# Kernel tuning notes

Hardware: AMD Instinct MI355X
Metric: run time of the kernel (lower is better)

## Reference

```python
import jax, jax.numpy as jnp
import numpy as np

NUM_USERS = 100000
NUM_ITEMS = 50000
N_NODES = NUM_USERS + NUM_ITEMS
EMB = 64          # emb_dim == layers[0]
NNZ = 2_400_000   # ~16 avg degree normalized-Laplacian nonzeros
BATCH = 16384


def spmm(rows, cols, vals, x, n):
    # sparse (COO) Laplacian @ dense features: out[r] += v * x[c]
    return jax.ops.segment_sum(vals[:, None] * x[cols], rows, num_segments=n)


def setup_inputs() -> dict:
    key = jax.random.key(0)
    ks = jax.random.split(key, 20)
    userIdx = jax.random.randint(ks[0], (BATCH,), 0, NUM_USERS)
    itemIdx = jax.random.randint(ks[1], (BATCH,), 0, NUM_ITEMS)
    lap_rows = jax.random.randint(ks[2], (NNZ,), 0, N_NODES, dtype=jnp.int32)
    lap_cols = jax.random.randint(ks[3], (NNZ,), 0, N_NODES, dtype=jnp.int32)
    # normalized Laplacian values ~ 1/sqrt(deg_i*deg_j), small positive
    lap_vals = jax.random.uniform(ks[4], (NNZ,), dtype=jnp.float32) * 0.05
    uEmb = jax.random.normal(ks[5], (NUM_USERS, EMB), dtype=jnp.float32) * 0.1
    iEmb = jax.random.normal(ks[6], (NUM_ITEMS, EMB), dtype=jnp.float32) * 0.1
    s = 1.0 / np.sqrt(EMB)
    gW0 = jax.random.normal(ks[7], (EMB, EMB), dtype=jnp.float32) * s
    gb0 = jnp.zeros((EMB,), jnp.float32)
    gW1 = jax.random.normal(ks[8], (EMB, EMB), dtype=jnp.float32) * s
    gb1 = jnp.zeros((EMB,), jnp.float32)
    D_CAT = EMB * 3 * 2  # 384
    W1 = jax.random.normal(ks[9], (D_CAT, 64), dtype=jnp.float32) / np.sqrt(D_CAT)
    b1 = jnp.zeros((64,), jnp.float32)
    W2 = jax.random.normal(ks[10], (64, 32), dtype=jnp.float32) / 8.0
    b2 = jnp.zeros((32,), jnp.float32)
    W3 = jax.random.normal(ks[11], (32, 1), dtype=jnp.float32) / np.sqrt(32.0)
    b3 = jnp.zeros((1,), jnp.float32)
    return {"userIdx": userIdx, "itemIdx": itemIdx,
            "lap_rows": lap_rows, "lap_cols": lap_cols, "lap_vals": lap_vals,
            "uEmb": uEmb, "iEmb": iEmb,
            "gW0": gW0, "gb0": gb0, "gW1": gW1, "gb1": gb1,
            "W1": W1, "b1": b1, "W2": W2, "b2": b2, "W3": W3, "b3": b3}


def reference(userIdx, itemIdx, lap_rows, lap_cols, lap_vals,
              uEmb, iEmb, gW0, gb0, gW1, gb1, W1, b1, W2, b2, W3, b3):
    features = jnp.concatenate([uEmb, iEmb], axis=0)  # [N, EMB]
    final = features
    for W, b in ((gW0, gb0), (gW1, gb1)):
        # (Laplacian + selfLoop I) @ features, then linear + ReLU
        h = spmm(lap_rows, lap_cols, lap_vals, features, N_NODES) + features
        features = jax.nn.relu(h @ W + b)
        final = jnp.concatenate([final, features], axis=1)
    u = final[userIdx]                     # [B, 192]
    it = final[itemIdx + NUM_USERS]        # [B, 192]
    e = jnp.concatenate([u, it], axis=1)   # [B, 384]
    e = jax.nn.relu(e @ W1 + b1)
    e = e @ W2 + b2
    e = e @ W3 + b3
    return e.ravel()
```

## Files before the change

### kernel.cpp

```cpp
#include <hip/hip_runtime.h>
#include <hip/hip_bf16.h>

#define NUM_USERS 100000
#define NUM_ITEMS 50000
#define N_NODES   150000
#define EMB       64
#define NNZ       2400000
#define BATCH     16384
#define D_CAT     384
#define BSHIFT    8
#define NBUCK     ((N_NODES + 255) >> 8)
#define EPB       9375

__device__ __forceinline__ unsigned short f2bf(float f) {
    unsigned u = __float_as_uint(f);
    unsigned r = u + 0x7fffu + ((u >> 16) & 1u);
    return (unsigned short)(r >> 16);
}
__device__ __forceinline__ float bflo(unsigned u) { return __uint_as_float(u << 16); }
__device__ __forceinline__ float bfhi(unsigned u) { return __uint_as_float(u & 0xffff0000u); }

__global__ __launch_bounds__(1024) void bucket_hist(const int* __restrict__ rows,
                                                    int* __restrict__ bcnt, int nnz) {
    __shared__ int h[NBUCK];
    int tid = threadIdx.x;
    for (int i = tid; i < NBUCK; i += 1024) h[i] = 0;
    __syncthreads();
    for (int i = blockIdx.x * 1024 + tid; i < nnz; i += gridDim.x * 1024)
        atomicAdd(&h[rows[i] >> BSHIFT], 1);
    __syncthreads();
    for (int i = tid; i < NBUCK; i += 1024) {
        int c = h[i];
        if (c) atomicAdd(&bcnt[i], c);
    }
}

__global__ __launch_bounds__(1024) void bucket_scan(const int* __restrict__ bcnt,
                                                    int* __restrict__ boffs,
                                                    int* __restrict__ gtails, int nnz) {
    __shared__ int s[1024];
    int t = threadIdx.x;
    int x = (t < NBUCK) ? bcnt[t] : 0;
    s[t] = x;
    __syncthreads();
#pragma unroll
    for (int off = 1; off < 1024; off <<= 1) {
        int v = (t >= off) ? s[t - off] : 0;
        __syncthreads();
        s[t] += v;
        __syncthreads();
    }
    if (t < NBUCK) {
        int e = s[t] - x;
        boffs[t] = e;
        gtails[t] = e;
    }
    if (t == 0) boffs[NBUCK] = nnz;
}

__global__ __launch_bounds__(1024) void coarse_multisplit(const int* __restrict__ rows,
                                                          const int* __restrict__ cols,
                                                          const float* __restrict__ vals,
                                                          int* __restrict__ gtails,
                                                          int2* __restrict__ pv, int nnz) {
    extern __shared__ int dyn[];
    int2* stage = (int2*)dyn;
    int*  smap  = dyn + 2 * EPB;
    __shared__ int hcnt[NBUCK];
    __shared__ int lstart[NBUCK];
    __shared__ int shiftv[NBUCK];

    int tid = threadIdx.x;
    int e0 = blockIdx.x * EPB;
    int e1 = e0 + EPB < nnz ? e0 + EPB : nnz;
    int nE = e1 - e0;

    for (int i = tid; i < NBUCK; i += 1024) hcnt[i] = 0;
    __syncthreads();
    for (int i = e0 + tid; i < e1; i += 1024)
        atomicAdd(&hcnt[rows[i] >> BSHIFT], 1);
    __syncthreads();

    int cnt = (tid < NBUCK) ? hcnt[tid] : 0;
    smap[tid] = cnt;
    __syncthreads();
#pragma unroll
    for (int off = 1; off < 1024; off <<= 1) {
        int v = (tid >= off) ? smap[tid - off] : 0;
        __syncthreads();
        smap[tid] += v;
        __syncthreads();
    }
    if (tid < NBUCK) {
        int ls = smap[tid] - cnt;
        lstart[tid] = ls;
        hcnt[tid] = ls;
        int gb = cnt ? atomicAdd(&gtails[tid], cnt) : 0;
        shiftv[tid] = gb - ls;
    }
    __syncthreads();

    for (int b = tid; b < NBUCK; b += 1024) {
        int beg = lstart[b];
        int end_ = (b == NBUCK - 1) ? nE : lstart[b + 1];
        int sh = shiftv[b];
        for (int k = beg; k < end_; ++k) smap[k] = sh;
    }
    __syncthreads();

    for (int i = e0 + tid; i < e1; i += 1024) {
        int r = rows[i];
        int p = atomicAdd(&hcnt[r >> BSHIFT], 1);
        stage[p] = make_int2(((r & 255) << 18) | cols[i], __float_as_int(vals[i]));
    }
    __syncthreads();

    for (int j = tid; j < nE; j += 1024)
        pv[smap[j] + j] = stage[j];
}

__global__ __launch_bounds__(1024) void fine_scatter(const int* __restrict__ boffs,
                                                     const int2* __restrict__ pv,
                                                     int2* __restrict__ packed,
                                                     int* __restrict__ row_ptr, int nnz) {
    __shared__ int rcnt[256];
    __shared__ int loff[256];
    int b = blockIdx.x;
    int tid = threadIdx.x;
    int lo = boffs[b], hi = boffs[b + 1];
    int r0 = b << BSHIFT;
    int nr = N_NODES - r0; if (nr > 256) nr = 256;

    if (tid < 256) rcnt[tid] = 0;
    __syncthreads();
    for (int i = lo + tid; i < hi; i += 1024)
        atomicAdd(&rcnt[pv[i].x >> 18], 1);
    __syncthreads();
    if (tid < 256) loff[tid] = rcnt[tid];
    __syncthreads();
#pragma unroll
    for (int off = 1; off < 256; off <<= 1) {
        int v = (tid < 256 && tid >= off) ? loff[tid - off] : 0;
        __syncthreads();
        if (tid < 256) loff[tid] += v;
        __syncthreads();
    }
    if (tid < 256) {
        int e = lo + loff[tid] - rcnt[tid];
        loff[tid] = e;
        if (tid < nr) row_ptr[r0 + tid] = e;
    }
    if (b == 0 && tid == 0) row_ptr[N_NODES] = nnz;
    __syncthreads();
    for (int i = lo + tid; i < hi; i += 1024) {
        int2 e = pv[i];
        int rl = e.x >> 18;
        int pos = atomicAdd(&loff[rl], 1);
        packed[pos] = make_int2(e.x & 0x3FFFF, e.y);
    }
}

__global__ __launch_bounds__(256) void gemm_table_f32(const float* __restrict__ uE,
                                                      const float* __restrict__ iE,
                                                      const float* __restrict__ W,
                                                      unsigned short* __restrict__ Zh,
                                                      int n_rows) {
    __shared__ float Wl[64 * 64];
    __shared__ float Xf[64 * 64];
    int tid = threadIdx.x;
    int lane = tid & 63;
    int wave = tid >> 6;
    int r0 = blockIdx.x * 64;
    int last = n_rows - 1;

    for (int i = tid; i < 64 * 64; i += 256) Wl[i] = W[i];
    for (int i = tid; i < 64 * 16; i += 256) {
        int row = i >> 4, q = i & 15;
        int r = r0 + row; r = r > last ? last : r;
        const float4* src = (r < NUM_USERS)
            ? (const float4*)(uE + (size_t)r * 64)
            : (const float4*)(iE + (size_t)(r - NUM_USERS) * 64);
        ((float4*)Xf)[i] = src[q];
    }
    __syncthreads();

    int rbase = wave * 16;
    float acc[16];
#pragma unroll
    for (int i = 0; i < 16; ++i) acc[i] = 0.f;

#pragma unroll 1
    for (int kc = 0; kc < 16; ++kc) {
        float w0 = Wl[(kc * 4 + 0) * 64 + lane];
        float w1 = Wl[(kc * 4 + 1) * 64 + lane];
        float w2 = Wl[(kc * 4 + 2) * 64 + lane];
        float w3 = Wl[(kc * 4 + 3) * 64 + lane];
#pragma unroll
        for (int i = 0; i < 16; ++i) {
            float4 q = ((const float4*)Xf)[(rbase + i) * 16 + kc];
            acc[i] = fmaf(q.x, w0, acc[i]);
            acc[i] = fmaf(q.y, w1, acc[i]);
            acc[i] = fmaf(q.z, w2, acc[i]);
            acc[i] = fmaf(q.w, w3, acc[i]);
        }
    }
#pragma unroll
    for (int i = 0; i < 16; ++i) {
        int r = r0 + rbase + i;
        if (r < n_rows) Zh[(size_t)r * 64 + lane] = f2bf(acc[i]);
    }
}

__global__ __launch_bounds__(256) void gemm_table_bf16(const unsigned* __restrict__ Xh,
                                                       const float* __restrict__ W,
                                                       unsigned short* __restrict__ Zh,
                                                       int n_rows) {
    __shared__ float Wl[64 * 64];
    __shared__ uint4 Xl4[64 * 8];
    int tid = threadIdx.x;
    int lane = tid & 63;
    int wave = tid >> 6;
    int r0 = blockIdx.x * 64;
    int nr = n_rows - r0; if (nr > 64) nr = 64;

    for (int i = tid; i < 64 * 64; i += 256) Wl[i] = W[i];
    const uint4* Xg4 = (const uint4*)(Xh + (size_t)r0 * 32);
    for (int i = tid; i < nr * 8; i += 256) Xl4[i] = Xg4[i];
    __syncthreads();

    const unsigned* Xl = (const unsigned*)Xl4;
    int rbase = wave * 16;
    float acc[16];
#pragma unroll
    for (int i = 0; i < 16; ++i) acc[i] = 0.f;

#pragma unroll 1
    for (int kc = 0; kc < 8; ++kc) {
        float w0 = Wl[(kc * 8 + 0) * 64 + lane];
        float w1 = Wl[(kc * 8 + 1) * 64 + lane];
        float w2 = Wl[(kc * 8 + 2) * 64 + lane];
        float w3 = Wl[(kc * 8 + 3) * 64 + lane];
        float w4 = Wl[(kc * 8 + 4) * 64 + lane];
        float w5 = Wl[(kc * 8 + 5) * 64 + lane];
        float w6 = Wl[(kc * 8 + 6) * 64 + lane];
        float w7 = Wl[(kc * 8 + 7) * 64 + lane];
#pragma unroll
        for (int i = 0; i < 16; ++i) {
            uint4 q = *(const uint4*)&Xl[(rbase + i) * 32 + kc * 4];
            acc[i] = fmaf(bflo(q.x), w0, acc[i]);
            acc[i] = fmaf(bfhi(q.x), w1, acc[i]);
            acc[i] = fmaf(bflo(q.y), w2, acc[i]);
            acc[i] = fmaf(bfhi(q.y), w3, acc[i]);
            acc[i] = fmaf(bflo(q.z), w4, acc[i]);
            acc[i] = fmaf(bfhi(q.z), w5, acc[i]);
            acc[i] = fmaf(bflo(q.w), w6, acc[i]);
            acc[i] = fmaf(bfhi(q.w), w7, acc[i]);
        }
    }
#pragma unroll
    for (int i = 0; i < 16; ++i) {
        int r = r0 + rbase + i;
        if (r < n_rows) Zh[(size_t)r * 64 + lane] = f2bf(acc[i]);
    }
}

__global__ __launch_bounds__(256) void spmm_bias_relu(const int* __restrict__ row_ptr,
                                                      const int2* __restrict__ packed,
                                                      const uint2* __restrict__ zh2,
                                                      const float* __restrict__ bias,
                                                      uint2* __restrict__ outh2,
                                                      int n_rows) {
    int tid = threadIdx.x;
    int lane = tid & 63;
    int wave = tid >> 6;
    int q = lane >> 4;
    int k = lane & 15;
    int r = blockIdx.x * 4 + wave;
    if (r >= n_rows) return;

    uint2 su = zh2[(size_t)r * 16 + k];
    float4 acc;
    acc.x = q ? 0.f : bflo(su.x);
    acc.y = q ? 0.f : bfhi(su.x);
    acc.z = q ? 0.f : bflo(su.y);
    acc.w = q ? 0.f : bfhi(su.y);

    int e = row_ptr[r] + q;
    int end = row_ptr[r + 1];
    for (; e + 13 < end; e += 16) {
        int2 p0 = packed[e + 0];
        int2 p1 = packed[e + 4];
        int2 p2 = packed[e + 8];
        int2 p3 = packed[e + 12];
        uint2 z0 = zh2[(size_t)p0.x * 16 + k];
        uint2 z1 = zh2[(size_t)p1.x * 16 + k];
        uint2 z2 = zh2[(size_t)p2.x * 16 + k];
        uint2 z3 = zh2[(size_t)p3.x * 16 + k];
        float v0 = __int_as_float(p0.y), v1 = __int_as_float(p1.y);
        float v2 = __int_as_float(p2.y), v3 = __int_as_float(p3.y);
        acc.x = fmaf(v0, bflo(z0.x), acc.x); acc.y = fmaf(v0, bfhi(z0.x), acc.y);
        acc.z = fmaf(v0, bflo(z0.y), acc.z); acc.w = fmaf(v0, bfhi(z0.y), acc.w);
        acc.x = fmaf(v1, bflo(z1.x), acc.x); acc.y = fmaf(v1, bfhi(z1.x), acc.y);
        acc.z = fmaf(v1, bflo(z1.y), acc.z); acc.w = fmaf(v1, bfhi(z1.y), acc.w);
        acc.x = fmaf(v2, bflo(z2.x), acc.x); acc.y = fmaf(v2, bfhi(z2.x), acc.y);
        acc.z = fmaf(v2, bflo(z2.y), acc.z); acc.w = fmaf(v2, bfhi(z2.y), acc.w);
        acc.x = fmaf(v3, bflo(z3.x), acc.x); acc.y = fmaf(v3, bfhi(z3.x), acc.y);
        acc.z = fmaf(v3, bflo(z3.y), acc.z); acc.w = fmaf(v3, bfhi(z3.y), acc.w);
    }
    for (; e < end; e += 4) {
        int2 p = packed[e];
        uint2 z = zh2[(size_t)p.x * 16 + k];
        float v = __int_as_float(p.y);
        acc.x = fmaf(v, bflo(z.x), acc.x); acc.y = fmaf(v, bfhi(z.x), acc.y);
        acc.z = fmaf(v, bflo(z.y), acc.z); acc.w = fmaf(v, bfhi(z.y), acc.w);
    }

    acc.x += __shfl_xor(acc.x, 16, 64);
    acc.y += __shfl_xor(acc.y, 16, 64);
    acc.z += __shfl_xor(acc.z, 16, 64);
    acc.w += __shfl_xor(acc.w, 16, 64);
    acc.x += __shfl_xor(acc.x, 32, 64);
    acc.y += __shfl_xor(acc.y, 32, 64);
    acc.z += __shfl_xor(acc.z, 32, 64);
    acc.w += __shfl_xor(acc.w, 32, 64);
    if (q == 0) {
        float4 bv = ((const float4*)bias)[k];
        float a = fmaxf(acc.x + bv.x, 0.f);
        float b = fmaxf(acc.y + bv.y, 0.f);
        float c = fmaxf(acc.z + bv.z, 0.f);
        float d = fmaxf(acc.w + bv.w, 0.f);
        outh2[(size_t)r * 16 + k] = make_uint2(
            ((unsigned)f2bf(b) << 16) | (unsigned)f2bf(a),
            ((unsigned)f2bf(d) << 16) | (unsigned)f2bf(c));
    }
}

__global__ __launch_bounds__(1024) void fused_mlp(
        const int* __restrict__ userIdx, const int* __restrict__ itemIdx,
        const float* __restrict__ uEmb, const float* __restrict__ iEmb,
        const unsigned short* __restrict__ feat1h,
        const unsigned short* __restrict__ feat2h,
        const float* __restrict__ W1, const float* __restrict__ b1,
        const float* __restrict__ W2, const float* __restrict__ b2,
        const float* __restrict__ W3, const float* __restrict__ b3,
        float* __restrict__ out) {
    __shared__ float    Wl[128 * 64];
    __shared__ unsigned El[64 * 64];
    __shared__ float    Ht[64 * 64];
    __shared__ float    W2l[64 * 32];
    __shared__ float    w3l[32];
    __shared__ float    b2l[32];
    __shared__ int      uidx[64], iidx[64];
    int tid = threadIdx.x;
    int lane = tid & 63;
    int wave = tid >> 6;
    int r0 = blockIdx.x * 64;
    int rbase = wave * 4;

    if (tid < 64) uidx[tid] = userIdx[r0 + tid];
    else if (tid < 128) iidx[tid - 64] = itemIdx[r0 + tid - 64];
    if (tid < 32) { w3l[tid] = W3[tid]; b2l[tid] = b2[tid]; }
    for (int i = tid; i < 64 * 32; i += 1024) W2l[i] = W2[i];

    float acc[4];
    float bv = b1[lane];
#pragma unroll
    for (int i = 0; i < 4; ++i) acc[i] = bv;

#pragma unroll 1
    for (int c = 0; c < 3; ++c) {
        __syncthreads();
        for (int i = tid; i < 128 * 64; i += 1024) Wl[i] = W1[c * 128 * 64 + i];
        {
            int t = tid;
            int row = t >> 4;
            int seg = (t >> 3) & 1;
            int q   = t & 7;
            int gseg = c * 2 + seg;
            uint4 val;
            if (gseg == 0 || gseg == 3) {
                const float* p = (gseg == 0)
                    ? uEmb + (size_t)uidx[row] * 64 + q * 8
                    : iEmb + (size_t)iidx[row] * 64 + q * 8;
                float4 a = *(const float4*)p;
                float4 b = *(const float4*)(p + 4);
                val.x = ((unsigned)f2bf(a.y) << 16) | f2bf(a.x);
                val.y = ((unsigned)f2bf(a.w) << 16) | f2bf(a.z);
                val.z = ((unsigned)f2bf(b.y) << 16) | f2bf(b.x);
                val.w = ((unsigned)f2bf(b.w) << 16) | f2bf(b.z);
            } else {
                const unsigned short* src;
                if (gseg == 1)      src = feat1h + (size_t)uidx[row] * 64;
                else if (gseg == 2) src = feat2h + (size_t)uidx[row] * 64;
                else if (gseg == 4) src = feat1h + (size_t)(iidx[row] + NUM_USERS) * 64;
                else                src = feat2h + (size_t)(iidx[row] + NUM_USERS) * 64;
                val = *(const uint4*)(src + q * 8);
            }
            *(uint4*)&El[row * 64 + seg * 32 + q * 4] = val;
        }
        __syncthreads();
        const uint4* El4 = (const uint4*)El;
#pragma unroll 1
        for (int k = 0; k < 128; k += 8) {
            float w0 = Wl[(k + 0) * 64 + lane];
            float w1 = Wl[(k + 1) * 64 + lane];
            float w2 = Wl[(k + 2) * 64 + lane];
            float w3 = Wl[(k + 3) * 64 + lane];
            float w4 = Wl[(k + 4) * 64 + lane];
            float w5 = Wl[(k + 5) * 64 + lane];
            float w6 = Wl[(k + 6) * 64 + lane];
            float w7 = Wl[(k + 7) * 64 + lane];
#pragma unroll
            for (int i = 0; i < 4; ++i) {
                uint4 q = El4[(rbase + i) * 16 + (k >> 3)];
                acc[i] = fmaf(bflo(q.x), w0, acc[i]);
                acc[i] = fmaf(bfhi(q.x), w1, acc[i]);
                acc[i] = fmaf(bflo(q.y), w2, acc[i]);
                acc[i] = fmaf(bfhi(q.y), w3, acc[i]);
                acc[i] = fmaf(bflo(q.z), w4, acc[i]);
                acc[i] = fmaf(bfhi(q.z), w5, acc[i]);
                acc[i] = fmaf(bflo(q.w), w6, acc[i]);
                acc[i] = fmaf(bfhi(q.w), w7, acc[i]);
            }
        }
    }

#pragma unroll
    for (int i = 0; i < 4; ++i) Ht[(rbase + i) * 64 + lane] = fmaxf(acc[i], 0.f);
    __syncthreads();

    int half = lane >> 5;
    int k = lane & 31;
    float b3v = b3[0];
#pragma unroll 1
    for (int p = 0; p < 2; ++p) {
        int row = rbase + p * 2 + half;
        float z = b2l[k];
#pragma unroll
        for (int j = 0; j < 64; ++j)
            z = fmaf(Ht[row * 64 + j], W2l[j * 32 + k], z);
        z *= w3l[k];
#pragma unroll
        for (int off = 16; off; off >>= 1)
            z += __shfl_xor(z, off, 64);
        if (k == 0) out[r0 + row] = z + b3v;
    }
}

extern "C" void kernel_launch(void* const* d_in, const int* in_sizes, int n_in,
                              void* d_out, int out_size, void* d_ws, size_t ws_size,
                              hipStream_t stream) {
    const int*   userIdx = (const int*)  d_in[0];
    const int*   itemIdx = (const int*)  d_in[1];
    const int*   lap_rows= (const int*)  d_in[2];
    const int*   lap_cols= (const int*)  d_in[3];
    const float* lap_vals= (const float*)d_in[4];
    const float* uEmb    = (const float*)d_in[5];
    const float* iEmb    = (const float*)d_in[6];
    const float* gW0     = (const float*)d_in[7];
    const float* gb0     = (const float*)d_in[8];
    const float* gW1     = (const float*)d_in[9];
    const float* gb1     = (const float*)d_in[10];
    const float* W1      = (const float*)d_in[11];
    const float* b1      = (const float*)d_in[12];
    const float* W2      = (const float*)d_in[13];
    const float* b2      = (const float*)d_in[14];
    const float* W3      = (const float*)d_in[15];
    const float* b3      = (const float*)d_in[16];
    float* out = (float*)d_out;

    const size_t NF = (size_t)N_NODES * EMB;
    char* w = (char*)d_ws;
    unsigned short* bufA = (unsigned short*)w;
    unsigned short* bufB = bufA + NF;
    char*  region3 = (char*)(bufB + NF);
    int2*  pv      = (int2*)region3;
    unsigned short* Zh = (unsigned short*)region3;
    int2*  packed  = (int2*)(region3 + NF * sizeof(float));
    int*   row_ptr = (int*)(packed + NNZ);
    int*   boffs   = row_ptr + (N_NODES + 1);
    int*   gtails  = boffs + (NBUCK + 1);
    int*   bcnt    = gtails + NBUCK;

    const int ms_grid   = (NNZ + EPB - 1) / EPB;
    const int ms_lds    = EPB * 12;
    const int spmm_grid = (N_NODES + 3) / 4;
    const int gemm_grid = (N_NODES + 63) / 64;

    hipMemsetAsync(bcnt, 0, NBUCK * sizeof(int), stream);
    bucket_hist<<<256, 1024, 0, stream>>>(lap_rows, bcnt, NNZ);
    bucket_scan<<<1, 1024, 0, stream>>>(bcnt, boffs, gtails, NNZ);
    coarse_multisplit<<<ms_grid, 1024, ms_lds, stream>>>(lap_rows, lap_cols, lap_vals,
                                                         gtails, pv, NNZ);
    fine_scatter<<<NBUCK, 1024, 0, stream>>>(boffs, pv, packed, row_ptr, NNZ);

    gemm_table_f32<<<gemm_grid, 256, 0, stream>>>(uEmb, iEmb, gW0, Zh, N_NODES);
    spmm_bias_relu<<<spmm_grid, 256, 0, stream>>>(row_ptr, packed, (const uint2*)Zh,
                                                  gb0, (uint2*)bufA, N_NODES);

    gemm_table_bf16<<<gemm_grid, 256, 0, stream>>>((const unsigned*)bufA, gW1, Zh, N_NODES);
    spmm_bias_relu<<<spmm_grid, 256, 0, stream>>>(row_ptr, packed, (const uint2*)Zh,
                                                  gb1, (uint2*)bufB, N_NODES);

    fused_mlp<<<BATCH / 64, 1024, 0, stream>>>(userIdx, itemIdx, uEmb, iEmb,
                                               bufA, bufB, W1, b1, W2, b2, W3, b3, out);
}
```

Before: 456.7 us.

## Fuse layer-1 SpMM epilogue with layer-2 dense transform into one kernel

Adds a kernel that runs the first SpMM with bias and ReLU, then immediately multiplies each output row by gW1 using register-held weights and readlane broadcasts, writing the next layer's Z table to a separate tail buffer. This removes the separate gemm_table_bf16 launch and its re-read of bufA. Each wave now processes 16 rows sequentially with 64 weight registers per thread, which lowers the number of waves in flight for the latency-bound gather. The fused path is used only when the workspace has room for the extra buffer.

Result: slower. 502.8 us (+10.1%).

```diff
diff --git a/kernel.cpp b/kernel.cpp
--- a/kernel.cpp
+++ b/kernel.cpp
@@ -332,6 +332,101 @@
         outh2[(size_t)r * 16 + k] = make_uint2(
             ((unsigned)f2bf(b) << 16) | (unsigned)f2bf(a),
             ((unsigned)f2bf(d) << 16) | (unsigned)f2bf(c));
+    }
+}
+
+__global__ __launch_bounds__(256) void spmm_bias_relu_z(const int* __restrict__ row_ptr,
+                                                        const int2* __restrict__ packed,
+                                                        const uint2* __restrict__ zh2,
+                                                        const float* __restrict__ bias,
+                                                        uint2* __restrict__ outh2,
+                                                        const float* __restrict__ Wz,
+                                                        unsigned short* __restrict__ Zh_out,
+                                                        int n_rows) {
+    int tid = threadIdx.x;
+    int lane = tid & 63;
+    int wave = tid >> 6;
+    int q = lane >> 4;
+    int k = lane & 15;
+
+    float wreg[64];
+#pragma unroll
+    for (int j = 0; j < 64; ++j) wreg[j] = Wz[j * 64 + lane];
+
+    float4 bv = ((const float4*)bias)[k];
+    int rbase = (blockIdx.x * 4 + wave) * 16;
+
+#pragma unroll 1
+    for (int ii = 0; ii < 16; ++ii) {
+        int r = rbase + ii;
+        if (r >= n_rows) break;
+
+        uint2 su = zh2[(size_t)r * 16 + k];
+        float4 acc;
+        acc.x = q ? 0.f : bflo(su.x);
+        acc.y = q ? 0.f : bfhi(su.x);
+        acc.z = q ? 0.f : bflo(su.y);
+        acc.w = q ? 0.f : bfhi(su.y);
+
+        int e = row_ptr[r] + q;
+        int end = row_ptr[r + 1];
+        for (; e + 13 < end; e += 16) {
+            int2 p0 = packed[e + 0];
+            int2 p1 = packed[e + 4];
+            int2 p2 = packed[e + 8];
+            int2 p3 = packed[e + 12];
+            uint2 z0 = zh2[(size_t)p0.x * 16 + k];
+            uint2 z1 = zh2[(size_t)p1.x * 16 + k];
+            uint2 z2 = zh2[(size_t)p2.x * 16 + k];
+            uint2 z3 = zh2[(size_t)p3.x * 16 + k];
+            float v0 = __int_as_float(p0.y), v1 = __int_as_float(p1.y);
+            float v2 = __int_as_float(p2.y), v3 = __int_as_float(p3.y);
+            acc.x = fmaf(v0, bflo(z0.x), acc.x); acc.y = fmaf(v0, bfhi(z0.x), acc.y);
+            acc.z = fmaf(v0, bflo(z0.y), acc.z); acc.w = fmaf(v0, bfhi(z0.y), acc.w);
+            acc.x = fmaf(v1, bflo(z1.x), acc.x); acc.y = fmaf(v1, bfhi(z1.x), acc.y);
+            acc.z = fmaf(v1, bflo(z1.y), acc.z); acc.w = fmaf(v1, bfhi(z1.y), acc.w);
+            acc.x = fmaf(v2, bflo(z2.x), acc.x); acc.y = fmaf(v2, bfhi(z2.x), acc.y);
+            acc.z = fmaf(v2, bflo(z2.y), acc.z); acc.w = fmaf(v2, bfhi(z2.y), acc.w);
+            acc.x = fmaf(v3, bflo(z3.x), acc.x); acc.y = fmaf(v3, bfhi(z3.x), acc.y);
+            acc.z = fmaf(v3, bflo(z3.y), acc.z); acc.w = fmaf(v3, bfhi(z3.y), acc.w);
+        }
+        for (; e < end; e += 4) {
+            int2 p = packed[e];
+            uint2 z = zh2[(size_t)p.x * 16 + k];
+            float v = __int_as_float(p.y);
+            acc.x = fmaf(v, bflo(z.x), acc.x); acc.y = fmaf(v, bfhi(z.x), acc.y);
+            acc.z = fmaf(v, bflo(z.y), acc.z); acc.w = fmaf(v, bfhi(z.y), acc.w);
+        }
+
+        acc.x += __shfl_xor(acc.x, 16, 64);
+        acc.y += __shfl_xor(acc.y, 16, 64);
+        acc.z += __shfl_xor(acc.z, 16, 64);
+        acc.w += __shfl_xor(acc.w, 16, 64);
+        acc.x += __shfl_xor(acc.x, 32, 64);
+        acc.y += __shfl_xor(acc.y, 32, 64);
+        acc.z += __shfl_xor(acc.z, 32, 64);
+        acc.w += __shfl_xor(acc.w, 32, 64);
+
+        float a = fmaxf(acc.x + bv.x, 0.f);
+        float b = fmaxf(acc.y + bv.y, 0.f);
+        float c = fmaxf(acc.z + bv.z, 0.f);
+        float d = fmaxf(acc.w + bv.w, 0.f);
+        int pa = (int)(((unsigned)f2bf(b) << 16) | (unsigned)f2bf(a));
+        int pb = (int)(((unsigned)f2bf(d) << 16) | (unsigned)f2bf(c));
+        if (q == 0)
+            outh2[(size_t)r * 16 + k] = make_uint2((unsigned)pa, (unsigned)pb);
+
+        float z = 0.f;
+#pragma unroll
+        for (int jj = 0; jj < 16; ++jj) {
+            unsigned ua = (unsigned)__builtin_amdgcn_readlane(pa, jj);
+            unsigned ub = (unsigned)__builtin_amdgcn_readlane(pb, jj);
+            z = fmaf(bflo(ua), wreg[4 * jj + 0], z);
+            z = fmaf(bfhi(ua), wreg[4 * jj + 1], z);
+            z = fmaf(bflo(ub), wreg[4 * jj + 2], z);
+            z = fmaf(bfhi(ub), wreg[4 * jj + 3], z);
+        }
+        Zh_out[(size_t)r * 64 + lane] = f2bf(z);
     }
 }
 
@@ -481,10 +576,14 @@
     int*   boffs   = row_ptr + (N_NODES + 1);
     int*   gtails  = boffs + (NBUCK + 1);
     int*   bcnt    = gtails + NBUCK;
+    size_t tail_off = ((size_t)((char*)(bcnt + NBUCK) - w) + 15) & ~(size_t)15;
+    unsigned short* Zh2 = (unsigned short*)(w + tail_off);
+    bool fuse = (tail_off + NF * sizeof(unsigned short)) <= ws_size;
 
     const int ms_grid   = (NNZ + EPB - 1) / EPB;
     const int ms_lds    = EPB * 12;
     const int spmm_grid = (N_NODES + 3) / 4;
+    const int spmmz_grid= (N_NODES + 63) / 64;
     const int gemm_grid = (N_NODES + 63) / 64;
 
     hipMemsetAsync(bcnt, 0, NBUCK * sizeof(int), stream);
@@ -495,12 +594,20 @@
     fine_scatter<<<NBUCK, 1024, 0, stream>>>(boffs, pv, packed, row_ptr, NNZ);
 
     gemm_table_f32<<<gemm_grid, 256, 0, stream>>>(uEmb, iEmb, gW0, Zh, N_NODES);
-    spmm_bias_relu<<<spmm_grid, 256, 0, stream>>>(row_ptr, packed, (const uint2*)Zh,
-                                                  gb0, (uint2*)bufA, N_NODES);
-
-    gemm_table_bf16<<<gemm_grid, 256, 0, stream>>>((const unsigned*)bufA, gW1, Zh, N_NODES);
-    spmm_bias_relu<<<spmm_grid, 256, 0, stream>>>(row_ptr, packed, (const uint2*)Zh,
-                                                  gb1, (uint2*)bufB, N_NODES);
+
+    if (fuse) {
+        spmm_bias_relu_z<<<spmmz_grid, 256, 0, stream>>>(row_ptr, packed,
+            (const uint2*)Zh, gb0, (uint2*)bufA, gW1, Zh2, N_NODES);
+        spmm_bias_relu<<<spmm_grid, 256, 0, stream>>>(row_ptr, packed,
+            (const uint2*)Zh2, gb1, (uint2*)bufB, N_NODES);
+    } else {
+        spmm_bias_relu<<<spmm_grid, 256, 0, stream>>>(row_ptr, packed,
+            (const uint2*)Zh, gb0, (uint2*)bufA, N_NODES);
+        gemm_table_bf16<<<gemm_grid, 256, 0, stream>>>((const unsigned*)bufA, gW1,
+                                                       Zh, N_NODES);
+        spmm_bias_relu<<<spmm_grid, 256, 0, stream>>>(row_ptr, packed,
+            (const uint2*)Zh, gb1, (uint2*)bufB, N_NODES);
+    }
 
     fused_mlp<<<BATCH / 64, 1024, 0, stream>>>(userIdx, itemIdx, uEmb, iEmb,
                                                bufA, bufB, W1, b1, W2, b2, W3, b3, out);
```

## Hold weights in registers and broadcast inputs via readlane in table GEMMs

Applied to the files above, without the earlier changes.

Both dense 64x64 table GEMM kernels drop their shared-memory staging of W and the input rows. Each lane now keeps its column of W in 64 registers, each wave loads its own 16 input rows straight from global memory, and input elements reach all lanes through readlane broadcasts feeding scalar-operand FMAs. This removes LDS traffic and the block barrier. In exchange it raises VGPR pressure, serialises readlane/FMA chains, and every wave reloads all of W from global memory.

Measured after the change: 459.3 us. About the same (+0.6%).

```diff
diff --git a/kernel.cpp b/kernel.cpp
--- a/kernel.cpp
+++ b/kernel.cpp
@@ -160,107 +160,75 @@
     }
 }
 
-__global__ __launch_bounds__(256) void gemm_table_f32(const float* __restrict__ uE,
-                                                      const float* __restrict__ iE,
-                                                      const float* __restrict__ W,
-                                                      unsigned short* __restrict__ Zh,
-                                                      int n_rows) {
-    __shared__ float Wl[64 * 64];
-    __shared__ float Xf[64 * 64];
+__global__ __launch_bounds__(256, 3) void gemm_table_f32(const float* __restrict__ uE,
+                                                         const float* __restrict__ iE,
+                                                         const float* __restrict__ W,
+                                                         unsigned short* __restrict__ Zh,
+                                                         int n_rows) {
     int tid = threadIdx.x;
     int lane = tid & 63;
     int wave = tid >> 6;
-    int r0 = blockIdx.x * 64;
+    int r0 = blockIdx.x * 64 + wave * 16;
     int last = n_rows - 1;
 
-    for (int i = tid; i < 64 * 64; i += 256) Wl[i] = W[i];
-    for (int i = tid; i < 64 * 16; i += 256) {
-        int row = i >> 4, q = i & 15;
-        int r = r0 + row; r = r > last ? last : r;
-        const float4* src = (r < NUM_USERS)
-            ? (const float4*)(uE + (size_t)r * 64)
-            : (const float4*)(iE + (size_t)(r - NUM_USERS) * 64);
-        ((float4*)Xf)[i] = src[q];
-    }
-    __syncthreads();
-
-    int rbase = wave * 16;
-    float acc[16];
-#pragma unroll
-    for (int i = 0; i < 16; ++i) acc[i] = 0.f;
-
-#pragma unroll 1
-    for (int kc = 0; kc < 16; ++kc) {
-        float w0 = Wl[(kc * 4 + 0) * 64 + lane];
-        float w1 = Wl[(kc * 4 + 1) * 64 + lane];
-        float w2 = Wl[(kc * 4 + 2) * 64 + lane];
-        float w3 = Wl[(kc * 4 + 3) * 64 + lane];
-#pragma unroll
-        for (int i = 0; i < 16; ++i) {
-            float4 q = ((const float4*)Xf)[(rbase + i) * 16 + kc];
-            acc[i] = fmaf(q.x, w0, acc[i]);
-            acc[i] = fmaf(q.y, w1, acc[i]);
-            acc[i] = fmaf(q.z, w2, acc[i]);
-            acc[i] = fmaf(q.w, w3, acc[i]);
+    float wreg[64];
+#pragma unroll
+    for (int k = 0; k < 64; ++k) wreg[k] = W[k * 64 + lane];
+
+    float x[16];
+#pragma unroll
+    for (int i = 0; i < 16; ++i) {
+        int r = r0 + i; r = r > last ? last : r;
+        x[i] = (r < NUM_USERS) ? uE[(size_t)r * 64 + lane]
+                               : iE[(size_t)(r - NUM_USERS) * 64 + lane];
+    }
+
+#pragma unroll
+    for (int i = 0; i < 16; ++i) {
+        float acc = 0.f;
+        int xb = __float_as_int(x[i]);
+#pragma unroll
+        for (int k = 0; k < 64; ++k) {
+            float xv = __int_as_float(__builtin_amdgcn_readlane(xb, k));
+            acc = fmaf(xv, wreg[k], acc);
         }
-    }
-#pragma unroll
-    for (int i = 0; i < 16; ++i) {
-        int r = r0 + rbase + i;
-        if (r < n_rows) Zh[(size_t)r * 64 + lane] = f2bf(acc[i]);
-    }
-}
-
-__global__ __launch_bounds__(256) void gemm_table_bf16(const unsigned* __restrict__ Xh,
-                                                       const float* __restrict__ W,
-                                                       unsigned short* __restrict__ Zh,
-                                                       int n_rows) {
-    __shared__ float Wl[64 * 64];
-    __shared__ uint4 Xl4[64 * 8];
+        int r = r0 + i;
+        if (r < n_rows) Zh[(size_t)r * 64 + lane] = f2bf(acc);
+    }
+}
+
+__global__ __launch_bounds__(256, 3) void gemm_table_bf16(const unsigned* __restrict__ Xh,
+                                                          const float* __restrict__ W,
+                                                          unsigned short* __restrict__ Zh,
+                                                          int n_rows) {
     int tid = threadIdx.x;
     int lane = tid & 63;
     int wave = tid >> 6;
-    int r0 = blockIdx.x * 64;
-    int nr = n_rows - r0; if (nr > 64) nr = 64;
-
-    for (int i = tid; i < 64 * 64; i += 256) Wl[i] = W[i];
-    const uint4* Xg4 = (const uint4*)(Xh + (size_t)r0 * 32);
-    for (int i = tid; i < nr * 8; i += 256) Xl4[i] = Xg4[i];
-    __syncthreads();
-
-    const unsigned* Xl = (const unsigned*)Xl4;
-    int rbase = wave * 16;
-    float acc[16];
-#pragma unroll
-    for (int i = 0; i < 16; ++i) acc[i] = 0.f;
-
-#pragma unroll 1
-    for (int kc = 0; kc < 8; ++kc) {
-        float w0 = Wl[(kc * 8 + 0) * 64 + lane];
-        float w1 = Wl[(kc * 8 + 1) * 64 + lane];
-        float w2 = Wl[(kc * 8 + 2) * 64 + lane];
-        float w3 = Wl[(kc * 8 + 3) * 64 + lane];
-        float w4 = Wl[(kc * 8 + 4) * 64 + lane];
-        float w5 = Wl[(kc * 8 + 5) * 64 + lane];
-        float w6 = Wl[(kc * 8 + 6) * 64 + lane];
-        float w7 = Wl[(kc * 8 + 7) * 64 + lane];
-#pragma unroll
-        for (int i = 0; i < 16; ++i) {
-            uint4 q = *(const uint4*)&Xl[(rbase + i) * 32 + kc * 4];
-            acc[i] = fmaf(bflo(q.x), w0, acc[i]);
-            acc[i] = fmaf(bfhi(q.x), w1, acc[i]);
-            acc[i] = fmaf(bflo(q.y), w2, acc[i]);
-            acc[i] = fmaf(bfhi(q.y), w3, acc[i]);
-            acc[i] = fmaf(bflo(q.z), w4, acc[i]);
-            acc[i] = fmaf(bfhi(q.z), w5, acc[i]);
-            acc[i] = fmaf(bflo(q.w), w6, acc[i]);
-            acc[i] = fmaf(bfhi(q.w), w7, acc[i]);
+    int r0 = blockIdx.x * 64 + wave * 16;
+    int last = n_rows - 1;
+
+    float wreg[64];
+#pragma unroll
+    for (int k = 0; k < 64; ++k) wreg[k] = W[k * 64 + lane];
+
+    unsigned x[16];
+#pragma unroll
+    for (int i = 0; i < 16; ++i) {
+        int r = r0 + i; r = r > last ? last : r;
+        x[i] = Xh[(size_t)r * 32 + (lane & 31)];
+    }
+
+#pragma unroll
+    for (int i = 0; i < 16; ++i) {
+        float acc = 0.f;
+#pragma unroll
+        for (int j = 0; j < 32; ++j) {
+            unsigned u = (unsigned)__builtin_amdgcn_readlane((int)x[i], j);
+            acc = fmaf(bflo(u), wreg[2 * j + 0], acc);
+            acc = fmaf(bfhi(u), wreg[2 * j + 1], acc);
         }
-    }
-#pragma unroll
-    for (int i = 0; i < 16; ++i) {
-        int r = r0 + rbase + i;
-        if (r < n_rows) Zh[(size_t)r * 64 + lane] = f2bf(acc[i]);
+        int r = r0 + i;
+        if (r < n_rows) Zh[(size_t)r * 64 + lane] = f2bf(acc);
     }
 }
 
```
